# Kernel optimization log

Hardware: AMD Instinct MI355X
Metric: run time of the kernel (lower is better)

## Reference

```python
import jax, jax.numpy as jnp
import numpy as np

B, N, DIM = 4, 384, 256


def setup_inputs() -> dict:
    key = jax.random.key(0)
    ks = jax.random.split(key, 8)
    sx = 1.0 / np.sqrt(DIM)
    si = 1.0  # Linear(1, dim): fan_in = 1
    return {
        "x": jax.random.normal(ks[0], (B, N, DIM), dtype=jnp.float32),
        "inc": jax.random.normal(ks[1], (B, N, N), dtype=jnp.float32),
        "Wx": jax.random.uniform(ks[2], (DIM, DIM), jnp.float32, -sx, sx),
        "bx": jax.random.uniform(ks[3], (DIM,), jnp.float32, -sx, sx),
        "Wi": jax.random.uniform(ks[4], (DIM,), jnp.float32, -si, si),  # Linear(1,dim) weight squeezed
        "bi": jax.random.uniform(ks[5], (DIM,), jnp.float32, -si, si),
        "Ws": jax.random.uniform(ks[6], (DIM,), jnp.float32, -sx, sx),  # Linear(dim,1) weight squeezed
        "bs": jax.random.uniform(ks[7], (1,), jnp.float32, -sx, sx),
    }


def reference(x, inc, Wx, bx, Wi, bi, Ws, bs):
    # proj_x: [B,N,dim]
    xp = jnp.einsum("bnd,ed->bne", x, Wx) + bx
    # proj_i on inc[...,None]: [B,N,N,dim]
    incp = inc[..., None] * Wi + bi
    # broadcast pairwise add: s[b,i,j,:] = xp[b,j] + xp[b,i] + incp[b,i,j]
    s = jax.nn.relu(xp[:, None, :, :] + xp[:, :, None, :] + incp)
    # proj_s to scalar + sigmoid: [B,N,N,1]
    logits = jnp.einsum("bijd,d->bij", s, Ws)[..., None] + bs
    return jax.nn.sigmoid(logits)
```

## Files before the change

### kernel.cpp

```cpp
#include <hip/hip_runtime.h>
#include <hip/hip_fp16.h>

#define DIM 256
#define NN  384

typedef _Float16 v2h __attribute__((ext_vector_type(2)));

__device__ __forceinline__ float fdot2f(__half2 a, __half2 b, float c) {
    return __builtin_amdgcn_fdot2(__builtin_bit_cast(v2h, a),
                                  __builtin_bit_cast(v2h, b), c, false);
}

__device__ __forceinline__ __half2 relu2(__half2 a) {
    v2h av = __builtin_bit_cast(v2h, a);
#if __has_builtin(__builtin_elementwise_max)
    v2h zv = {(_Float16)0.0f, (_Float16)0.0f};
    v2h rv = __builtin_elementwise_max(av, zv);
#else
    v2h rv;
    rv.x = av.x > (_Float16)0.0f ? av.x : (_Float16)0.0f;
    rv.y = av.y > (_Float16)0.0f ? av.y : (_Float16)0.0f;
#endif
    return __builtin_bit_cast(__half2, rv);
}

__global__ __launch_bounds__(256) void k_transpose(const float* __restrict__ W,
                                                   float* __restrict__ WT,
                                                   const float* __restrict__ Wi,
                                                   const float* __restrict__ Ws,
                                                   __half* __restrict__ wih,
                                                   __half* __restrict__ wsh) {
    __shared__ float t[32][33];
    const int bx = blockIdx.x & 7, by = blockIdx.x >> 3;
    const int tx = threadIdx.x & 31, ty = threadIdx.x >> 5;
#pragma unroll
    for (int k = 0; k < 4; k++) {
        const int r = ty + k * 8;
        t[r][tx] = W[(by * 32 + r) * DIM + bx * 32 + tx];
    }
    if (blockIdx.x == 0) {
        wih[threadIdx.x] = __float2half(Wi[threadIdx.x]);
        wsh[threadIdx.x] = __float2half(Ws[threadIdx.x]);
    }
    __syncthreads();
#pragma unroll
    for (int k = 0; k < 4; k++) {
        const int r = ty + k * 8;
        WT[(bx * 32 + r) * DIM + by * 32 + tx] = t[tx][r];
    }
}

#define PR 4
__global__ __launch_bounds__(256) void k_proj(const float* __restrict__ x,
                                              const float* __restrict__ WxT,
                                              const float* __restrict__ bx,
                                              const float* __restrict__ bi,
                                              __half* __restrict__ xph,
                                              __half* __restrict__ xpbh) {
    __shared__ float xs[PR][DIM];
    const int row0 = blockIdx.x * PR;
    const int e = threadIdx.x;
    const float* xr = x + (size_t)row0 * DIM;
#pragma unroll
    for (int k = 0; k < PR; k++) xs[k][e] = xr[k * DIM + e];
    __syncthreads();

    float acc[PR];
    const float b0 = bx[e];
#pragma unroll
    for (int r = 0; r < PR; r++) acc[r] = b0;

    float w0 = WxT[0 * DIM + e];
    float w1 = WxT[1 * DIM + e];
    float w2 = WxT[2 * DIM + e];
    float w3 = WxT[3 * DIM + e];
    for (int d = 0; d < DIM; d += 4) {
        const int dn = (d + 4) & (DIM - 1);
        const float n0 = WxT[(dn + 0) * DIM + e];
        const float n1 = WxT[(dn + 1) * DIM + e];
        const float n2 = WxT[(dn + 2) * DIM + e];
        const float n3 = WxT[(dn + 3) * DIM + e];
#pragma unroll
        for (int r = 0; r < PR; r++) {
            const float4 xv = *(const float4*)&xs[r][d];
            acc[r] = fmaf(xv.x, w0, acc[r]);
            acc[r] = fmaf(xv.y, w1, acc[r]);
            acc[r] = fmaf(xv.z, w2, acc[r]);
            acc[r] = fmaf(xv.w, w3, acc[r]);
        }
        w0 = n0; w1 = n1; w2 = n2; w3 = n3;
    }
    const float biv = bi[e];
#pragma unroll
    for (int r = 0; r < PR; r++) {
        xph [(size_t)(row0 + r) * DIM + e] = __float2half(acc[r]);
        xpbh[(size_t)(row0 + r) * DIM + e] = __float2half(acc[r] + biv);
    }
}

#define LDW 264
__global__ __launch_bounds__(256) void k_main(const __half* __restrict__ xpbh,
                                              const __half* __restrict__ xph,
                                              const float* __restrict__ inc,
                                              const __half* __restrict__ wih,
                                              const __half* __restrict__ wsh,
                                              const float* __restrict__ bs,
                                              float* __restrict__ out) {
    __shared__ __half xi[32][LDW];
    __shared__ __half xj[32][LDW];
    const int blk = blockIdx.x;
    const int jt = blk % 12;
    const int it = (blk / 12) % 12;
    const int b  = blk / 144;
    const int i0 = it * 32, j0 = jt * 32;
    const int t  = threadIdx.x;
    const int il = t >> 4, jl = t & 15;

    const float* incp = inc + ((size_t)(b * NN) + i0 + il) * NN + j0 + jl;
    const float inc00 = incp[0];
    const float inc01 = incp[16];
    const float inc10 = incp[16 * NN];
    const float inc11 = incp[16 * NN + 16];
    const float bsv = bs[0];

    const __half* gi = xpbh + (size_t)(b * NN + i0) * DIM;
    const __half* gj = xph  + (size_t)(b * NN + j0) * DIM;
    for (int idx = t; idx < 32 * 32; idx += 256) {
        const int r = idx >> 5, c = (idx & 31) * 8;
        *(float4*)(&xi[r][c]) = *(const float4*)(gi + r * DIM + c);
        *(float4*)(&xj[r][c]) = *(const float4*)(gj + r * DIM + c);
    }
    __syncthreads();

    const __half2 i00p = __float2half2_rn(inc00);
    const __half2 i01p = __float2half2_rn(inc01);
    const __half2 i10p = __float2half2_rn(inc10);
    const __half2 i11p = __float2half2_rn(inc11);
    float a00 = bsv, a01 = bsv, a10 = bsv, a11 = bsv;

    const __half2* wih2 = (const __half2*)wih;
    const __half2* wsh2 = (const __half2*)wsh;

    union F4H { float4 f; __half2 h[4]; };
#pragma unroll
    for (int d = 0; d < DIM; d += 8) {
        F4H hi0, hi1, hj0, hj1;
        hi0.f = *(const float4*)&xi[il][d];
        hi1.f = *(const float4*)&xi[il + 16][d];
        hj0.f = *(const float4*)&xj[jl][d];
        hj1.f = *(const float4*)&xj[jl + 16][d];
#pragma unroll
        for (int k2 = 0; k2 < 4; k2++) {
            const __half2 wi2 = wih2[(d >> 1) + k2];
            const __half2 ws2 = wsh2[(d >> 1) + k2];
            __half2 s00 = __hadd2(hi0.h[k2], hj0.h[k2]);
            __half2 s01 = __hadd2(hi0.h[k2], hj1.h[k2]);
            __half2 s10 = __hadd2(hi1.h[k2], hj0.h[k2]);
            __half2 s11 = __hadd2(hi1.h[k2], hj1.h[k2]);
            s00 = __hfma2(i00p, wi2, s00);
            s01 = __hfma2(i01p, wi2, s01);
            s10 = __hfma2(i10p, wi2, s10);
            s11 = __hfma2(i11p, wi2, s11);
            s00 = relu2(s00);
            s01 = relu2(s01);
            s10 = relu2(s10);
            s11 = relu2(s11);
            a00 = fdot2f(s00, ws2, a00);
            a01 = fdot2f(s01, ws2, a01);
            a10 = fdot2f(s10, ws2, a10);
            a11 = fdot2f(s11, ws2, a11);
        }
    }
    float* op = out + ((size_t)(b * NN) + i0 + il) * NN + j0 + jl;
    op[0]            = 1.f / (1.f + __expf(-a00));
    op[16]           = 1.f / (1.f + __expf(-a01));
    op[16 * NN]      = 1.f / (1.f + __expf(-a10));
    op[16 * NN + 16] = 1.f / (1.f + __expf(-a11));
}

extern "C" void kernel_launch(void* const* d_in, const int* in_sizes, int n_in,
                              void* d_out, int out_size, void* d_ws, size_t ws_size,
                              hipStream_t stream) {
    const float* x   = (const float*)d_in[0];
    const float* inc = (const float*)d_in[1];
    const float* Wx  = (const float*)d_in[2];
    const float* bx  = (const float*)d_in[3];
    const float* Wi  = (const float*)d_in[4];
    const float* bi  = (const float*)d_in[5];
    const float* Ws  = (const float*)d_in[6];
    const float* bs  = (const float*)d_in[7];
    float* out = (float*)d_out;

    char* ws = (char*)d_ws;
    float*  WxT  = (float*)ws;
    __half* xph  = (__half*)(ws + 262144);
    __half* xpbh = (__half*)(ws + 262144 + 786432);
    __half* wih  = (__half*)(ws + 262144 + 2 * 786432);
    __half* wsh  = (__half*)(ws + 262144 + 2 * 786432 + 512);

    k_transpose<<<64,  256, 0, stream>>>(Wx, WxT, Wi, Ws, wih, wsh);
    k_proj     <<<384, 256, 0, stream>>>(x, WxT, bx, bi, xph, xpbh);
    k_main     <<<576, 256, 0, stream>>>(xpbh, xph, inc, wih, wsh, bs, out);
}
```

Baseline: 96.54 us.

## Drop transpose kernel, stage Wx chunks in LDS, enlarge main tile to 48x48

Removes the separate transpose launch. The projection kernel now loads Wx row-chunks into padded shared memory with register prefetch and does six rows per block. The main kernel grows each tile from 32x32 to 48x48, so each thread computes 3x3 outputs with software-pipelined LDS loads for more reuse. The trade-off is that the grid shrinks to 256 blocks, which may leave part of the device idle, and register use rises.

```diff
diff --git a/kernel.cpp b/kernel.cpp
--- a/kernel.cpp
+++ b/kernel.cpp
@@ -24,77 +24,75 @@
     return __builtin_bit_cast(__half2, rv);
 }
 
-__global__ __launch_bounds__(256) void k_transpose(const float* __restrict__ W,
-                                                   float* __restrict__ WT,
-                                                   const float* __restrict__ Wi,
-                                                   const float* __restrict__ Ws,
-                                                   __half* __restrict__ wih,
-                                                   __half* __restrict__ wsh) {
-    __shared__ float t[32][33];
-    const int bx = blockIdx.x & 7, by = blockIdx.x >> 3;
-    const int tx = threadIdx.x & 31, ty = threadIdx.x >> 5;
-#pragma unroll
-    for (int k = 0; k < 4; k++) {
-        const int r = ty + k * 8;
-        t[r][tx] = W[(by * 32 + r) * DIM + bx * 32 + tx];
-    }
-    if (blockIdx.x == 0) {
-        wih[threadIdx.x] = __float2half(Wi[threadIdx.x]);
-        wsh[threadIdx.x] = __float2half(Ws[threadIdx.x]);
-    }
-    __syncthreads();
-#pragma unroll
-    for (int k = 0; k < 4; k++) {
-        const int r = ty + k * 8;
-        WT[(bx * 32 + r) * DIM + by * 32 + tx] = t[tx][r];
-    }
-}
-
-#define PR 4
+#define PRJ  6
+#define WCH  32
+#define WPAD 36
 __global__ __launch_bounds__(256) void k_proj(const float* __restrict__ x,
-                                              const float* __restrict__ WxT,
+                                              const float* __restrict__ Wx,
                                               const float* __restrict__ bx,
                                               const float* __restrict__ bi,
+                                              const float* __restrict__ Wi,
+                                              const float* __restrict__ Ws,
                                               __half* __restrict__ xph,
-                                              __half* __restrict__ xpbh) {
-    __shared__ float xs[PR][DIM];
-    const int row0 = blockIdx.x * PR;
-    const int e = threadIdx.x;
+                                              __half* __restrict__ xpbh,
+                                              __half* __restrict__ wih,
+                                              __half* __restrict__ wsh) {
+    __shared__ float wl[DIM][WPAD];
+    const int t  = threadIdx.x;
+    const int r0 = t >> 3;
+    const int c4 = t & 7;
+    const int row0 = blockIdx.x * PRJ;
     const float* xr = x + (size_t)row0 * DIM;
-#pragma unroll
-    for (int k = 0; k < PR; k++) xs[k][e] = xr[k * DIM + e];
-    __syncthreads();
-
-    float acc[PR];
-    const float b0 = bx[e];
-#pragma unroll
-    for (int r = 0; r < PR; r++) acc[r] = b0;
-
-    float w0 = WxT[0 * DIM + e];
-    float w1 = WxT[1 * DIM + e];
-    float w2 = WxT[2 * DIM + e];
-    float w3 = WxT[3 * DIM + e];
-    for (int d = 0; d < DIM; d += 4) {
-        const int dn = (d + 4) & (DIM - 1);
-        const float n0 = WxT[(dn + 0) * DIM + e];
-        const float n1 = WxT[(dn + 1) * DIM + e];
-        const float n2 = WxT[(dn + 2) * DIM + e];
-        const float n3 = WxT[(dn + 3) * DIM + e];
-#pragma unroll
-        for (int r = 0; r < PR; r++) {
-            const float4 xv = *(const float4*)&xs[r][d];
-            acc[r] = fmaf(xv.x, w0, acc[r]);
-            acc[r] = fmaf(xv.y, w1, acc[r]);
-            acc[r] = fmaf(xv.z, w2, acc[r]);
-            acc[r] = fmaf(xv.w, w3, acc[r]);
-        }
-        w0 = n0; w1 = n1; w2 = n2; w3 = n3;
-    }
-    const float biv = bi[e];
-#pragma unroll
-    for (int r = 0; r < PR; r++) {
-        xph [(size_t)(row0 + r) * DIM + e] = __float2half(acc[r]);
-        xpbh[(size_t)(row0 + r) * DIM + e] = __float2half(acc[r] + biv);
+
+    if (blockIdx.x == 0) {
+        wih[t] = __float2half(Wi[t]);
+        wsh[t] = __float2half(Ws[t]);
+    }
+
+    const float* wsrc = Wx + c4 * 4;
+    float4 pf[8];
+#pragma unroll
+    for (int k = 0; k < 8; k++)
+        pf[k] = *(const float4*)(wsrc + (size_t)(r0 + 32 * k) * DIM);
+
+    float acc[PRJ];
+    const float bxe = bx[t];
+#pragma unroll
+    for (int r = 0; r < PRJ; r++) acc[r] = bxe;
+
+#pragma unroll 1
+    for (int c = 0; c < 8; c++) {
+        if (c) __syncthreads();
+#pragma unroll
+        for (int k = 0; k < 8; k++)
+            *(float4*)&wl[r0 + 32 * k][c4 * 4] = pf[k];
+        __syncthreads();
+        if (c < 7) {
+            const float* nsrc = wsrc + (c + 1) * WCH;
+#pragma unroll
+            for (int k = 0; k < 8; k++)
+                pf[k] = *(const float4*)(nsrc + (size_t)(r0 + 32 * k) * DIM);
+        }
+        const int d0 = c * WCH;
+#pragma unroll
+        for (int q = 0; q < 8; q++) {
+            const float4 wv = *(const float4*)&wl[t][q * 4];
+#pragma unroll
+            for (int r = 0; r < PRJ; r++) {
+                const float4 xv = *(const float4*)(xr + r * DIM + d0 + q * 4);
+                acc[r] = fmaf(wv.x, xv.x, acc[r]);
+                acc[r] = fmaf(wv.y, xv.y, acc[r]);
+                acc[r] = fmaf(wv.z, xv.z, acc[r]);
+                acc[r] = fmaf(wv.w, xv.w, acc[r]);
+            }
+        }
+    }
+
+    const float biv = bi[t];
+#pragma unroll
+    for (int r = 0; r < PRJ; r++) {
+        xph [(size_t)(row0 + r) * DIM + t] = __float2half(acc[r]);
+        xpbh[(size_t)(row0 + r) * DIM + t] = __float2half(acc[r] + biv);
     }
 }
 
@@ -106,76 +104,88 @@
                                               const __half* __restrict__ wsh,
                                               const float* __restrict__ bs,
                                               float* __restrict__ out) {
-    __shared__ __half xi[32][LDW];
-    __shared__ __half xj[32][LDW];
+    __shared__ __half xi[48][LDW];
+    __shared__ __half xj[48][LDW];
     const int blk = blockIdx.x;
-    const int jt = blk % 12;
-    const int it = (blk / 12) % 12;
-    const int b  = blk / 144;
-    const int i0 = it * 32, j0 = jt * 32;
+    const int jt = blk & 7;
+    const int it = (blk >> 3) & 7;
+    const int b  = blk >> 6;
+    const int i0 = it * 48, j0 = jt * 48;
     const int t  = threadIdx.x;
     const int il = t >> 4, jl = t & 15;
 
     const float* incp = inc + ((size_t)(b * NN) + i0 + il) * NN + j0 + jl;
-    const float inc00 = incp[0];
-    const float inc01 = incp[16];
-    const float inc10 = incp[16 * NN];
-    const float inc11 = incp[16 * NN + 16];
+    float incv[3][3];
+#pragma unroll
+    for (int a = 0; a < 3; a++)
+#pragma unroll
+        for (int c = 0; c < 3; c++)
+            incv[a][c] = incp[(size_t)(a * 16) * NN + c * 16];
     const float bsv = bs[0];
 
     const __half* gi = xpbh + (size_t)(b * NN + i0) * DIM;
     const __half* gj = xph  + (size_t)(b * NN + j0) * DIM;
-    for (int idx = t; idx < 32 * 32; idx += 256) {
+    for (int idx = t; idx < 48 * 32; idx += 256) {
         const int r = idx >> 5, c = (idx & 31) * 8;
         *(float4*)(&xi[r][c]) = *(const float4*)(gi + r * DIM + c);
         *(float4*)(&xj[r][c]) = *(const float4*)(gj + r * DIM + c);
     }
     __syncthreads();
 
-    const __half2 i00p = __float2half2_rn(inc00);
-    const __half2 i01p = __float2half2_rn(inc01);
-    const __half2 i10p = __float2half2_rn(inc10);
-    const __half2 i11p = __float2half2_rn(inc11);
-    float a00 = bsv, a01 = bsv, a10 = bsv, a11 = bsv;
+    __half2 ip[3][3];
+    float acc[3][3];
+#pragma unroll
+    for (int a = 0; a < 3; a++)
+#pragma unroll
+        for (int c = 0; c < 3; c++) {
+            ip[a][c]  = __float2half2_rn(incv[a][c]);
+            acc[a][c] = bsv;
+        }
 
     const __half2* wih2 = (const __half2*)wih;
     const __half2* wsh2 = (const __half2*)wsh;
 
     union F4H { float4 f; __half2 h[4]; };
-#pragma unroll
+    F4H hi[3], hj[3];
+#pragma unroll
+    for (int a = 0; a < 3; a++) {
+        hi[a].f = *(const float4*)&xi[il + 16 * a][0];
+        hj[a].f = *(const float4*)&xj[jl + 16 * a][0];
+    }
+
+#pragma unroll 4
     for (int d = 0; d < DIM; d += 8) {
-        F4H hi0, hi1, hj0, hj1;
-        hi0.f = *(const float4*)&xi[il][d];
-        hi1.f = *(const float4*)&xi[il + 16][d];
-        hj0.f = *(const float4*)&xj[jl][d];
-        hj1.f = *(const float4*)&xj[jl + 16][d];
+        const int dn = (d + 8) & (DIM - 1);
+        F4H ni[3], nj[3];
+#pragma unroll
+        for (int a = 0; a < 3; a++) {
+            ni[a].f = *(const float4*)&xi[il + 16 * a][dn];
+            nj[a].f = *(const float4*)&xj[jl + 16 * a][dn];
+        }
 #pragma unroll
         for (int k2 = 0; k2 < 4; k2++) {
             const __half2 wi2 = wih2[(d >> 1) + k2];
             const __half2 ws2 = wsh2[(d >> 1) + k2];
-            __half2 s00 = __hadd2(hi0.h[k2], hj0.h[k2]);
-            __half2 s01 = __hadd2(hi0.h[k2], hj1.h[k2]);
-            __half2 s10 = __hadd2(hi1.h[k2], hj0.h[k2]);
-            __half2 s11 = __hadd2(hi1.h[k2], hj1.h[k2]);
-            s00 = __hfma2(i00p, wi2, s00);
-            s01 = __hfma2(i01p, wi2, s01);
-            s10 = __hfma2(i10p, wi2, s10);
-            s11 = __hfma2(i11p, wi2, s11);
-            s00 = relu2(s00);
-            s01 = relu2(s01);
-            s10 = relu2(s10);
-            s11 = relu2(s11);
-            a00 = fdot2f(s00, ws2, a00);
-            a01 = fdot2f(s01, ws2, a01);
-            a10 = fdot2f(s10, ws2, a10);
-            a11 = fdot2f(s11, ws2, a11);
-        }
-    }
+#pragma unroll
+            for (int a = 0; a < 3; a++)
+#pragma unroll
+                for (int c = 0; c < 3; c++) {
+                    __half2 s = __hadd2(hi[a].h[k2], hj[c].h[k2]);
+                    s = __hfma2(ip[a][c], wi2, s);
+                    s = relu2(s);
+                    acc[a][c] = fdot2f(s, ws2, acc[a][c]);
+                }
+        }
+#pragma unroll
+        for (int a = 0; a < 3; a++) { hi[a] = ni[a]; hj[a] = nj[a]; }
+    }
+
     float* op = out + ((size_t)(b * NN) + i0 + il) * NN + j0 + jl;
-    op[0]            = 1.f / (1.f + __expf(-a00));
-    op[16]           = 1.f / (1.f + __expf(-a01));
-    op[16 * NN]      = 1.f / (1.f + __expf(-a10));
-    op[16 * NN + 16] = 1.f / (1.f + __expf(-a11));
+#pragma unroll
+    for (int a = 0; a < 3; a++)
+#pragma unroll
+        for (int c = 0; c < 3; c++)
+            op[(size_t)(a * 16) * NN + c * 16] = 1.f / (1.f + __expf(-acc[a][c]));
 }
 
 extern "C" void kernel_launch(void* const* d_in, const int* in_sizes, int n_in,
@@ -192,13 +202,11 @@
     float* out = (float*)d_out;
 
     char* ws = (char*)d_ws;
-    float*  WxT  = (float*)ws;
-    __half* xph  = (__half*)(ws + 262144);
-    __half* xpbh = (__half*)(ws + 262144 + 786432);
-    __half* wih  = (__half*)(ws + 262144 + 2 * 786432);
-    __half* wsh  = (__half*)(ws + 262144 + 2 * 786432 + 512);
-
-    k_transpose<<<64,  256, 0, stream>>>(Wx, WxT, Wi, Ws, wih, wsh);
-    k_proj     <<<384, 256, 0, stream>>>(x, WxT, bx, bi, xph, xpbh);
-    k_main     <<<576, 256, 0, stream>>>(xpbh, xph, inc, wih, wsh, bs, out);
-}
+    __half* xph  = (__half*)ws;
+    __half* xpbh = (__half*)(ws + 786432);
+    __half* wih  = (__half*)(ws + 2 * 786432);
+    __half* wsh  = (__half*)(ws + 2 * 786432 + 512);
+
+    k_proj<<<256, 256, 0, stream>>>(x, Wx, bx, bi, Wi, Ws, xph, xpbh, wih, wsh);
+    k_main<<<256, 256, 0, stream>>>(xpbh, xph, inc, wih, wsh, bs, out);
+}
```

New measurement: 124.6 us. 1.29x slower.

## Enlarge main kernel tile to 48x48 with 3x3 per-thread outputs and LDS prefetch

Applied to the files above, without the earlier changes.

Each thread now computes a 3x3 block of output pairs instead of 2x2, so blocks cover 48x48 (i,j) tiles and the grid shrinks to 256 blocks. This raises reuse of the shared-memory xi/xj loads per output and adds register double-buffering of the next d-slice. In exchange, register pressure rises and the grid has fewer blocks, which may leave compute units underoccupied and reduce latency hiding.

```diff
diff --git a/kernel.cpp b/kernel.cpp
--- a/kernel.cpp
+++ b/kernel.cpp
@@ -106,76 +106,88 @@
                                               const __half* __restrict__ wsh,
                                               const float* __restrict__ bs,
                                               float* __restrict__ out) {
-    __shared__ __half xi[32][LDW];
-    __shared__ __half xj[32][LDW];
+    __shared__ __half xi[48][LDW];
+    __shared__ __half xj[48][LDW];
     const int blk = blockIdx.x;
-    const int jt = blk % 12;
-    const int it = (blk / 12) % 12;
-    const int b  = blk / 144;
-    const int i0 = it * 32, j0 = jt * 32;
+    const int jt = blk & 7;
+    const int it = (blk >> 3) & 7;
+    const int b  = blk >> 6;
+    const int i0 = it * 48, j0 = jt * 48;
     const int t  = threadIdx.x;
     const int il = t >> 4, jl = t & 15;
 
     const float* incp = inc + ((size_t)(b * NN) + i0 + il) * NN + j0 + jl;
-    const float inc00 = incp[0];
-    const float inc01 = incp[16];
-    const float inc10 = incp[16 * NN];
-    const float inc11 = incp[16 * NN + 16];
+    float incv[3][3];
+#pragma unroll
+    for (int a = 0; a < 3; a++)
+#pragma unroll
+        for (int c = 0; c < 3; c++)
+            incv[a][c] = incp[(size_t)(a * 16) * NN + c * 16];
     const float bsv = bs[0];
 
     const __half* gi = xpbh + (size_t)(b * NN + i0) * DIM;
     const __half* gj = xph  + (size_t)(b * NN + j0) * DIM;
-    for (int idx = t; idx < 32 * 32; idx += 256) {
+    for (int idx = t; idx < 48 * 32; idx += 256) {
         const int r = idx >> 5, c = (idx & 31) * 8;
         *(float4*)(&xi[r][c]) = *(const float4*)(gi + r * DIM + c);
         *(float4*)(&xj[r][c]) = *(const float4*)(gj + r * DIM + c);
     }
     __syncthreads();
 
-    const __half2 i00p = __float2half2_rn(inc00);
-    const __half2 i01p = __float2half2_rn(inc01);
-    const __half2 i10p = __float2half2_rn(inc10);
-    const __half2 i11p = __float2half2_rn(inc11);
-    float a00 = bsv, a01 = bsv, a10 = bsv, a11 = bsv;
+    __half2 ip[3][3];
+    float acc[3][3];
+#pragma unroll
+    for (int a = 0; a < 3; a++)
+#pragma unroll
+        for (int c = 0; c < 3; c++) {
+            ip[a][c]  = __float2half2_rn(incv[a][c]);
+            acc[a][c] = bsv;
+        }
 
     const __half2* wih2 = (const __half2*)wih;
     const __half2* wsh2 = (const __half2*)wsh;
 
     union F4H { float4 f; __half2 h[4]; };
-#pragma unroll
+    F4H hi[3], hj[3];
+#pragma unroll
+    for (int a = 0; a < 3; a++) {
+        hi[a].f = *(const float4*)&xi[il + 16 * a][0];
+        hj[a].f = *(const float4*)&xj[jl + 16 * a][0];
+    }
+
+#pragma unroll 4
     for (int d = 0; d < DIM; d += 8) {
-        F4H hi0, hi1, hj0, hj1;
-        hi0.f = *(const float4*)&xi[il][d];
-        hi1.f = *(const float4*)&xi[il + 16][d];
-        hj0.f = *(const float4*)&xj[jl][d];
-        hj1.f = *(const float4*)&xj[jl + 16][d];
+        const int dn = (d + 8) & (DIM - 1);
+        F4H ni[3], nj[3];
+#pragma unroll
+        for (int a = 0; a < 3; a++) {
+            ni[a].f = *(const float4*)&xi[il + 16 * a][dn];
+            nj[a].f = *(const float4*)&xj[jl + 16 * a][dn];
+        }
 #pragma unroll
         for (int k2 = 0; k2 < 4; k2++) {
             const __half2 wi2 = wih2[(d >> 1) + k2];
             const __half2 ws2 = wsh2[(d >> 1) + k2];
-            __half2 s00 = __hadd2(hi0.h[k2], hj0.h[k2]);
-            __half2 s01 = __hadd2(hi0.h[k2], hj1.h[k2]);
-            __half2 s10 = __hadd2(hi1.h[k2], hj0.h[k2]);
-            __half2 s11 = __hadd2(hi1.h[k2], hj1.h[k2]);
-            s00 = __hfma2(i00p, wi2, s00);
-            s01 = __hfma2(i01p, wi2, s01);
-            s10 = __hfma2(i10p, wi2, s10);
-            s11 = __hfma2(i11p, wi2, s11);
-            s00 = relu2(s00);
-            s01 = relu2(s01);
-            s10 = relu2(s10);
-            s11 = relu2(s11);
-            a00 = fdot2f(s00, ws2, a00);
-            a01 = fdot2f(s01, ws2, a01);
-            a10 = fdot2f(s10, ws2, a10);
-            a11 = fdot2f(s11, ws2, a11);
-        }
-    }
+#pragma unroll
+            for (int a = 0; a < 3; a++)
+#pragma unroll
+                for (int c = 0; c < 3; c++) {
+                    __half2 s = __hadd2(hi[a].h[k2], hj[c].h[k2]);
+                    s = __hfma2(ip[a][c], wi2, s);
+                    s = relu2(s);
+                    acc[a][c] = fdot2f(s, ws2, acc[a][c]);
+                }
+        }
+#pragma unroll
+        for (int a = 0; a < 3; a++) { hi[a] = ni[a]; hj[a] = nj[a]; }
+    }
+
     float* op = out + ((size_t)(b * NN) + i0 + il) * NN + j0 + jl;
-    op[0]            = 1.f / (1.f + __expf(-a00));
-    op[16]           = 1.f / (1.f + __expf(-a01));
-    op[16 * NN]      = 1.f / (1.f + __expf(-a10));
-    op[16 * NN + 16] = 1.f / (1.f + __expf(-a11));
+#pragma unroll
+    for (int a = 0; a < 3; a++)
+#pragma unroll
+        for (int c = 0; c < 3; c++)
+            op[(size_t)(a * 16) * NN + c * 16] = 1.f / (1.f + __expf(-acc[a][c]));
 }
 
 extern "C" void kernel_launch(void* const* d_in, const int* in_sizes, int n_in,
@@ -200,5 +212,5 @@
 
     k_transpose<<<64,  256, 0, stream>>>(Wx, WxT, Wi, Ws, wih, wsh);
     k_proj     <<<384, 256, 0, stream>>>(x, WxT, bx, bi, xph, xpbh);
-    k_main     <<<576, 256, 0, stream>>>(xpbh, xph, inc, wih, wsh, bs, out);
-}
+    k_main     <<<256, 256, 0, stream>>>(xpbh, xph, inc, wih, wsh, bs, out);
+}
```

After: 99.07 us. 1.03x slower.
